# Performance work log

Measured on AMD Instinct MI355X. Metric: run time of the kernel, lower is better.

The kernel has to match this reference:

```python
import jax, jax.numpy as jnp
import numpy as np

Q, C, D = 4096, 4096, 1024
EPS = 1e-6  # torch.nn.PairwiseDistance default eps, added to (x1 - x2)


def _cdist_l2(a, b):
    # ||(a + EPS) - b||_2 for all pairs, via GEMM formulation.
    a = a + EPS
    sq = (jnp.sum(a * a, axis=1)[:, None]
          + jnp.sum(b * b, axis=1)[None, :]
          - 2.0 * a @ b.T)
    return jnp.sqrt(jnp.maximum(sq, 0.0))


def setup_inputs() -> dict:
    key = jax.random.key(0)
    k1, k2, k3, k4, k5, k6 = jax.random.split(key, 6)
    return {
        "context_rgb_features": jax.random.normal(k1, (C, D), dtype=jnp.float32),
        "context_flow_features": jax.random.normal(k2, (C, D), dtype=jnp.float32),
        "target_rgb_features": jax.random.normal(k3, (Q, D), dtype=jnp.float32),
        "target_flow_features": jax.random.normal(k4, (Q, D), dtype=jnp.float32),
        "c_r": jax.random.uniform(k5, (Q,), dtype=jnp.float32, minval=0.1, maxval=1.0),
        "c_f": jax.random.uniform(k6, (Q,), dtype=jnp.float32, minval=0.1, maxval=1.0),
    }


def reference(context_rgb_features, context_flow_features,
              target_rgb_features, target_flow_features, c_r, c_f):
    denom = c_r + c_f
    w_r = (c_r / denom)[:, None]   # [Q, 1]
    w_f = (c_f / denom)[:, None]
    d_rgb = _cdist_l2(target_rgb_features, context_rgb_features)    # [Q, C]
    d_flow = _cdist_l2(target_flow_features, context_flow_features)  # [Q, C]
    posterior = w_r * jnp.exp(-d_rgb) + w_f * jnp.exp(-d_flow)
    return posterior / jnp.sum(posterior, axis=1, keepdims=True)
```

## Files before the change

### kernel.cpp

```cpp
#include <hip/hip_runtime.h>
#include <hip/hip_bf16.h>

#define QN 4096
#define CN 4096
#define DN 1024
#define EPSV 1e-6f

#define BM 256
#define BN 256
#define TK 64
#define NT (DN / TK)
#define ATILE (BM * TK)
#define BUFE (2 * ATILE)

#define MATSZ ((size_t)QN * DN)

using bf16x8 = __attribute__((ext_vector_type(8))) __bf16;
using f32x4  = __attribute__((ext_vector_type(4))) float;

static __device__ __forceinline__ unsigned short f2bf_rne(float x) {
  unsigned int u = __float_as_uint(x);
  unsigned int r = (u + 0x7FFFu + ((u >> 16) & 1u)) >> 16;
  return (unsigned short)r;
}
static __device__ __forceinline__ float bf2f(unsigned short h) {
  return __uint_as_float(((unsigned int)h) << 16);
}

static __device__ __forceinline__ void gload_lds16(const unsigned short* g, unsigned short* l) {
  __builtin_amdgcn_global_load_lds(
      (const __attribute__((address_space(1))) unsigned int*)g,
      (__attribute__((address_space(3))) unsigned int*)l, 16, 0, 0);
}


__global__ void prep_kernel(const float* __restrict__ tgt_r, const float* __restrict__ tgt_f,
                            const float* __restrict__ ctx_r, const float* __restrict__ ctx_f,
                            unsigned short* __restrict__ ws16, float* __restrict__ norms) {
  const int row = blockIdx.x;
  const int mat = blockIdx.y;
  const int t = threadIdx.x;
  const float* src; float eps;
  switch (mat) {
    case 0:  src = tgt_r; eps = EPSV; break;
    case 1:  src = tgt_f; eps = EPSV; break;
    case 2:  src = ctx_r; eps = 0.f;  break;
    default: src = ctx_f; eps = 0.f;  break;
  }
  unsigned short* hi = ws16 + (size_t)mat * MATSZ;
  float* nrm = norms + (size_t)mat * QN;
  const size_t base = (size_t)row * DN;
  float4 v = ((const float4*)(src + base))[t];
  float a[4] = {v.x + eps, v.y + eps, v.z + eps, v.w + eps};
  float ss = 0.f;
  unsigned short hh[4];
#pragma unroll
  for (int k = 0; k < 4; ++k) {
    hh[k] = f2bf_rne(a[k]);
    float f = bf2f(hh[k]);
    ss += f * f;
  }
  ((ushort4*)(hi + base))[t] = make_ushort4(hh[0], hh[1], hh[2], hh[3]);
#pragma unroll
  for (int o = 32; o > 0; o >>= 1) ss += __shfl_down(ss, o);
  __shared__ float red[4];
  if ((t & 63) == 0) red[t >> 6] = ss;
  __syncthreads();
  if (t == 0) nrm[row] = red[0] + red[1] + red[2] + red[3];
}

template <bool ACCUM>
__global__ __launch_bounds__(512, 2)
void gemm_kernel(const unsigned short* __restrict__ A,
                 const unsigned short* __restrict__ B,
                 const float* __restrict__ tn,
                 const float* __restrict__ cn,
                 const float* __restrict__ cw_num,
                 const float* __restrict__ cw_oth,
                 float* __restrict__ out) {
  __shared__ unsigned short S[2 * BUFE];

  const int t = threadIdx.x;
  const int lane = t & 63;
  const int wid = t >> 6;
  const int wr = wid >> 2;
  const int wc = wid & 3;
  const int row0 = blockIdx.y * BM;
  const int col0 = blockIdx.x * BN;

  f32x4 acc[8][4];
#pragma unroll
  for (int m = 0; m < 8; ++m)
#pragma unroll
    for (int n = 0; n < 4; ++n)
      acc[m][n] = (f32x4){0.f, 0.f, 0.f, 0.f};

  const int srw = lane >> 3;
  const int sch = (lane & 7) ^ srw;
  const size_t src_off = (size_t)(wid * 8 + srw) * DN + sch * 8;
  const int ldsw = wid * 512;

  const unsigned short* pA = A + (size_t)row0 * DN + src_off;
  const unsigned short* pB = B + (size_t)col0 * DN + src_off;

  const int lr = lane & 15;
  const int lq = lane >> 4;
  const int sc0 = (lq ^ (lr & 7)) * 8;
  int ra[8], rb[4];
#pragma unroll
  for (int m = 0; m < 8; ++m) ra[m] = (wr * 128 + m * 16 + lr) * TK + sc0;
#pragma unroll
  for (int n = 0; n < 4; ++n) rb[n] = (wc * 64 + n * 16 + lr) * TK + sc0;
#define KS1(x) ((x) ^ 32)

#define STAGE(buf, kk)                                                        \
  do {                                                                        \
    unsigned short* Sb_ = S + (buf) * BUFE;                                   \
    _Pragma("unroll")                                                         \
    for (int i_ = 0; i_ < 4; ++i_) {                                          \
      const size_t g_ = (size_t)i_ * 64 * DN + (kk);                          \
      gload_lds16(pA + g_, Sb_ + i_ * 4096 + ldsw);                           \
      gload_lds16(pB + g_, Sb_ + ATILE + i_ * 4096 + ldsw);                   \
    }                                                                         \
  } while (0)

  STAGE(0, 0);
  __syncthreads();

  int cur = 0;
  for (int tt = 0; tt < NT; ++tt) {
    if (tt + 1 < NT) STAGE(cur ^ 1, (tt + 1) * TK);

    const unsigned short* Sb = S + cur * BUFE;
#pragma unroll
    for (int ksub = 0; ksub < 2; ++ksub) {
      bf16x8 a[8], b[4];
#pragma unroll
      for (int m = 0; m < 8; ++m)
        a[m] = *(const bf16x8*)(Sb + (ksub ? KS1(ra[m]) : ra[m]));
#pragma unroll
      for (int n = 0; n < 4; ++n)
        b[n] = *(const bf16x8*)(Sb + ATILE + (ksub ? KS1(rb[n]) : rb[n]));
#pragma unroll
      for (int m = 0; m < 8; ++m)
#pragma unroll
        for (int n = 0; n < 4; ++n)
          acc[m][n] = __builtin_amdgcn_mfma_f32_16x16x32_bf16(a[m], b[n], acc[m][n], 0, 0, 0);
    }

    __syncthreads();
    cur ^= 1;
  }

  float cnv[4];
  int ccv[4];
#pragma unroll
  for (int n = 0; n < 4; ++n) {
    ccv[n] = col0 + wc * 64 + n * 16 + lr;
    cnv[n] = cn[ccv[n]];
  }

#pragma unroll
  for (int m = 0; m < 8; ++m) {
#pragma unroll
    for (int r = 0; r < 4; ++r) {
      const int tq = row0 + wr * 128 + m * 16 + lq * 4 + r;
      const float tnq = tn[tq];
      const float num = cw_num[tq], oth = cw_oth[tq];
      const float wgt = num / (num + oth);
      float* orow = out + (size_t)tq * CN;
#pragma unroll
      for (int n = 0; n < 4; ++n) {
        const float sq = tnq + cnv[n] - 2.f * acc[m][n][r];
        const float d = sqrtf(fmaxf(sq, 0.f));
        const float e = wgt * __expf(-d);
        if (ACCUM) orow[ccv[n]] += e;
        else       orow[ccv[n]] = e;
      }
    }
  }
}

__global__ void norm_kernel(float* __restrict__ out) {
  const int row = blockIdx.x;
  const int t = threadIdx.x;
  float4* p = (float4*)(out + (size_t)row * CN);
  float4 v[4];
  float s = 0.f;
#pragma unroll
  for (int i = 0; i < 4; ++i) {
    v[i] = p[t + 256 * i];
    s += v[i].x + v[i].y + v[i].z + v[i].w;
  }
#pragma unroll
  for (int o = 32; o > 0; o >>= 1) s += __shfl_down(s, o);
  __shared__ float red[4];
  if ((t & 63) == 0) red[t >> 6] = s;
  __syncthreads();
  const float inv = 1.f / (red[0] + red[1] + red[2] + red[3]);
#pragma unroll
  for (int i = 0; i < 4; ++i) {
    v[i].x *= inv; v[i].y *= inv; v[i].z *= inv; v[i].w *= inv;
    p[t + 256 * i] = v[i];
  }
}

extern "C" void kernel_launch(void* const* d_in, const int* in_sizes, int n_in,
                              void* d_out, int out_size, void* d_ws, size_t ws_size,
                              hipStream_t stream) {
  const float* ctx_r = (const float*)d_in[0];
  const float* ctx_f = (const float*)d_in[1];
  const float* tgt_r = (const float*)d_in[2];
  const float* tgt_f = (const float*)d_in[3];
  const float* c_r   = (const float*)d_in[4];
  const float* c_f   = (const float*)d_in[5];
  float* out = (float*)d_out;
  unsigned short* ws16 = (unsigned short*)d_ws;
  float* norms = (float*)(ws16 + 4 * MATSZ);

  prep_kernel<<<dim3(QN, 4), 256, 0, stream>>>(tgt_r, tgt_f, ctx_r, ctx_f, ws16, norms);
  gemm_kernel<false><<<dim3(CN / BN, QN / BM), 512, 0, stream>>>(
      ws16 + 0 * MATSZ, ws16 + 2 * MATSZ, norms, norms + 2 * QN, c_r, c_f, out);
  gemm_kernel<true><<<dim3(CN / BN, QN / BM), 512, 0, stream>>>(
      ws16 + 1 * MATSZ, ws16 + 3 * MATSZ, norms + QN, norms + 3 * QN, c_f, c_r, out);
  norm_kernel<<<QN, 256, 0, stream>>>(out);
}
```

Baseline: 231.5 us.

## Split GEMM tile into quadrant sub-phases with interleaved half-tile prefetch

Restructures the bf16 MFMA main loop so each 256x256 block is computed as four 128x128 quadrants. Global-to-LDS loads of the next K-tile are issued as half-tiles between the quadrant phases, with explicit barriers, vmcnt/lgkmcnt waits, sched_barriers and setprio around the MFMA bursts. Each wave's 8x4 fragment layout becomes 2x2 quadrants of 4x2 fragments, which is meant to overlap LDS fills with compute and lower fragment register pressure. In exchange it adds many more barriers per K-tile and relies on hand-tuned wait counts for correctness.

```diff
diff --git a/kernel.cpp b/kernel.cpp
--- a/kernel.cpp
+++ b/kernel.cpp
@@ -8,10 +8,11 @@
 
 #define BM 256
 #define BN 256
-#define TK 64
-#define NT (DN / TK)
-#define ATILE (BM * TK)
-#define BUFE (2 * ATILE)
+#define BK 64
+#define NTILES (DN / BK)
+#define HALF 8192
+#define SLAB 16384
+#define BUF  32768
 
 #define MATSZ ((size_t)QN * DN)
 
@@ -78,107 +79,198 @@
                  const float* __restrict__ cw_num,
                  const float* __restrict__ cw_oth,
                  float* __restrict__ out) {
-  __shared__ unsigned short S[2 * BUFE];
+  __shared__ unsigned short S[2 * BUF];
 
   const int t = threadIdx.x;
   const int lane = t & 63;
   const int wid = t >> 6;
-  const int wr = wid >> 2;
-  const int wc = wid & 3;
+  const int wr2 = wid >> 2;
+  const int wc2 = wid & 3;
   const int row0 = blockIdx.y * BM;
   const int col0 = blockIdx.x * BN;
 
-  f32x4 acc[8][4];
-#pragma unroll
-  for (int m = 0; m < 8; ++m)
-#pragma unroll
-    for (int n = 0; n < 4; ++n)
-      acc[m][n] = (f32x4){0.f, 0.f, 0.f, 0.f};
+  f32x4 acc[2][2][4][2];
+#pragma unroll
+  for (int qa = 0; qa < 2; ++qa)
+#pragma unroll
+    for (int qb = 0; qb < 2; ++qb)
+#pragma unroll
+      for (int m = 0; m < 4; ++m)
+#pragma unroll
+        for (int n = 0; n < 2; ++n)
+          acc[qa][qb][m][n] = (f32x4){0.f, 0.f, 0.f, 0.f};
 
   const int srw = lane >> 3;
   const int sch = (lane & 7) ^ srw;
-  const size_t src_off = (size_t)(wid * 8 + srw) * DN + sch * 8;
-  const int ldsw = wid * 512;
-
-  const unsigned short* pA = A + (size_t)row0 * DN + src_off;
-  const unsigned short* pB = B + (size_t)col0 * DN + src_off;
+  const size_t so0 = (size_t)(wid * 8 + srw) * DN + sch * 8;
+  const size_t so1 = (size_t)(64 + wid * 8 + srw) * DN + sch * 8;
+  const int lo0 = (wid * 8) * 64;
+  const int lo1 = (64 + wid * 8) * 64;
+
+  const unsigned short* pA = A + (size_t)row0 * DN;
+  const unsigned short* pB = B + (size_t)col0 * DN;
 
   const int lr = lane & 15;
   const int lq = lane >> 4;
   const int sc0 = (lq ^ (lr & 7)) * 8;
-  int ra[8], rb[4];
-#pragma unroll
-  for (int m = 0; m < 8; ++m) ra[m] = (wr * 128 + m * 16 + lr) * TK + sc0;
-#pragma unroll
-  for (int n = 0; n < 4; ++n) rb[n] = (wc * 64 + n * 16 + lr) * TK + sc0;
-#define KS1(x) ((x) ^ 32)
-
-#define STAGE(buf, kk)                                                        \
+  int raoff[4][2], rboff[2][2];
+#pragma unroll
+  for (int m = 0; m < 4; ++m) {
+    const int base = (wr2 * 64 + m * 16 + lr) * BK + sc0;
+    raoff[m][0] = base; raoff[m][1] = base ^ 32;
+  }
+#pragma unroll
+  for (int n = 0; n < 2; ++n) {
+    const int base = (wc2 * 32 + n * 16 + lr) * BK + sc0;
+    rboff[n][0] = base; rboff[n][1] = base ^ 32;
+  }
+
+#define STAGEH(src, ldsbase, h, kk)                                           \
   do {                                                                        \
-    unsigned short* Sb_ = S + (buf) * BUFE;                                   \
-    _Pragma("unroll")                                                         \
-    for (int i_ = 0; i_ < 4; ++i_) {                                          \
-      const size_t g_ = (size_t)i_ * 64 * DN + (kk);                          \
-      gload_lds16(pA + g_, Sb_ + i_ * 4096 + ldsw);                           \
-      gload_lds16(pB + g_, Sb_ + ATILE + i_ * 4096 + ldsw);                   \
-    }                                                                         \
+    gload_lds16((src) + (size_t)((h) * 128) * DN + (kk) + so0,                \
+                (ldsbase) + (h) * HALF + lo0);                                \
+    gload_lds16((src) + (size_t)((h) * 128) * DN + (kk) + so1,                \
+                (ldsbase) + (h) * HALF + lo1);                                \
   } while (0)
 
-  STAGE(0, 0);
-  __syncthreads();
-
-  int cur = 0;
-  for (int tt = 0; tt < NT; ++tt) {
-    if (tt + 1 < NT) STAGE(cur ^ 1, (tt + 1) * TK);
-
-    const unsigned short* Sb = S + cur * BUFE;
-#pragma unroll
-    for (int ksub = 0; ksub < 2; ++ksub) {
-      bf16x8 a[8], b[4];
-#pragma unroll
-      for (int m = 0; m < 8; ++m)
-        a[m] = *(const bf16x8*)(Sb + (ksub ? KS1(ra[m]) : ra[m]));
-#pragma unroll
-      for (int n = 0; n < 4; ++n)
-        b[n] = *(const bf16x8*)(Sb + ATILE + (ksub ? KS1(rb[n]) : rb[n]));
-#pragma unroll
-      for (int m = 0; m < 8; ++m)
-#pragma unroll
-        for (int n = 0; n < 4; ++n)
-          acc[m][n] = __builtin_amdgcn_mfma_f32_16x16x32_bf16(a[m], b[n], acc[m][n], 0, 0, 0);
-    }
-
-    __syncthreads();
-    cur ^= 1;
-  }
-
-  float cnv[4];
-  int ccv[4];
-#pragma unroll
-  for (int n = 0; n < 4; ++n) {
-    ccv[n] = col0 + wc * 64 + n * 16 + lr;
-    cnv[n] = cn[ccv[n]];
-  }
-
-#pragma unroll
-  for (int m = 0; m < 8; ++m) {
-#pragma unroll
-    for (int r = 0; r < 4; ++r) {
-      const int tq = row0 + wr * 128 + m * 16 + lq * 4 + r;
-      const float tnq = tn[tq];
-      const float num = cw_num[tq], oth = cw_oth[tq];
-      const float wgt = num / (num + oth);
-      float* orow = out + (size_t)tq * CN;
-#pragma unroll
-      for (int n = 0; n < 4; ++n) {
-        const float sq = tnq + cnv[n] - 2.f * acc[m][n][r];
-        const float d = sqrtf(fmaxf(sq, 0.f));
-        const float e = wgt * __expf(-d);
-        if (ACCUM) orow[ccv[n]] += e;
-        else       orow[ccv[n]] = e;
-      }
-    }
-  }
+#define SBAR() __builtin_amdgcn_sched_barrier(0)
+#define BARRIER() do { SBAR(); __builtin_amdgcn_s_barrier(); SBAR(); } while (0)
+#define WAITLGKM0() do { asm volatile("s_waitcnt lgkmcnt(0)" ::: "memory"); SBAR(); } while (0)
+#define WAITVM4()   do { asm volatile("s_waitcnt vmcnt(4)" ::: "memory"); SBAR(); } while (0)
+
+  {
+    unsigned short* Na = S;
+    unsigned short* Nb = S + SLAB;
+    STAGEH(pA, Na, 0, 0);
+    STAGEH(pB, Nb, 0, 0);
+    STAGEH(pB, Nb, 1, 0);
+    STAGEH(pA, Na, 1, 0);
+    WAITVM4();
+    BARRIER();
+  }
+
+  bf16x8 Af[4][2], B0f[2][2], B1f[2][2];
+
+  for (int tt = 0; tt < NTILES; ++tt) {
+    const int b = tt & 1;
+    const unsigned short* Sa = S + b * BUF;
+    const unsigned short* Sb = S + b * BUF + SLAB;
+    unsigned short* Na = S + (b ^ 1) * BUF;
+    unsigned short* Nb = S + (b ^ 1) * BUF + SLAB;
+    const int kn = (tt + 1) * BK;
+    const bool notlast = (tt + 1 < NTILES);
+
+#pragma unroll
+    for (int m = 0; m < 4; ++m) {
+      Af[m][0] = *(const bf16x8*)(Sa + raoff[m][0]);
+      Af[m][1] = *(const bf16x8*)(Sa + raoff[m][1]);
+    }
+#pragma unroll
+    for (int n = 0; n < 2; ++n) {
+      B0f[n][0] = *(const bf16x8*)(Sb + rboff[n][0]);
+      B0f[n][1] = *(const bf16x8*)(Sb + rboff[n][1]);
+    }
+    if (notlast) STAGEH(pA, Na, 0, kn);
+    BARRIER();
+    WAITLGKM0();
+    __builtin_amdgcn_s_setprio(1);
+#pragma unroll
+    for (int m = 0; m < 4; ++m)
+#pragma unroll
+      for (int n = 0; n < 2; ++n) {
+        acc[0][0][m][n] = __builtin_amdgcn_mfma_f32_16x16x32_bf16(Af[m][0], B0f[n][0], acc[0][0][m][n], 0, 0, 0);
+        acc[0][0][m][n] = __builtin_amdgcn_mfma_f32_16x16x32_bf16(Af[m][1], B0f[n][1], acc[0][0][m][n], 0, 0, 0);
+      }
+    __builtin_amdgcn_s_setprio(0);
+    WAITVM4();
+    BARRIER();
+
+#pragma unroll
+    for (int n = 0; n < 2; ++n) {
+      B1f[n][0] = *(const bf16x8*)(Sb + HALF + rboff[n][0]);
+      B1f[n][1] = *(const bf16x8*)(Sb + HALF + rboff[n][1]);
+    }
+    if (notlast) STAGEH(pB, Nb, 0, kn);
+    BARRIER();
+    WAITLGKM0();
+    __builtin_amdgcn_s_setprio(1);
+#pragma unroll
+    for (int m = 0; m < 4; ++m)
+#pragma unroll
+      for (int n = 0; n < 2; ++n) {
+        acc[0][1][m][n] = __builtin_amdgcn_mfma_f32_16x16x32_bf16(Af[m][0], B1f[n][0], acc[0][1][m][n], 0, 0, 0);
+        acc[0][1][m][n] = __builtin_amdgcn_mfma_f32_16x16x32_bf16(Af[m][1], B1f[n][1], acc[0][1][m][n], 0, 0, 0);
+      }
+    __builtin_amdgcn_s_setprio(0);
+    WAITVM4();
+    BARRIER();
+
+#pragma unroll
+    for (int m = 0; m < 4; ++m) {
+      Af[m][0] = *(const bf16x8*)(Sa + HALF + raoff[m][0]);
+      Af[m][1] = *(const bf16x8*)(Sa + HALF + raoff[m][1]);
+    }
+    if (notlast) STAGEH(pB, Nb, 1, kn);
+    BARRIER();
+    WAITLGKM0();
+    __builtin_amdgcn_s_setprio(1);
+#pragma unroll
+    for (int m = 0; m < 4; ++m)
+#pragma unroll
+      for (int n = 0; n < 2; ++n) {
+        acc[1][1][m][n] = __builtin_amdgcn_mfma_f32_16x16x32_bf16(Af[m][0], B1f[n][0], acc[1][1][m][n], 0, 0, 0);
+        acc[1][1][m][n] = __builtin_amdgcn_mfma_f32_16x16x32_bf16(Af[m][1], B1f[n][1], acc[1][1][m][n], 0, 0, 0);
+      }
+    __builtin_amdgcn_s_setprio(0);
+    BARRIER();
+
+    if (notlast) STAGEH(pA, Na, 1, kn);
+    BARRIER();
+    __builtin_amdgcn_s_setprio(1);
+#pragma unroll
+    for (int m = 0; m < 4; ++m)
+#pragma unroll
+      for (int n = 0; n < 2; ++n) {
+        acc[1][0][m][n] = __builtin_amdgcn_mfma_f32_16x16x32_bf16(Af[m][0], B0f[n][0], acc[1][0][m][n], 0, 0, 0);
+        acc[1][0][m][n] = __builtin_amdgcn_mfma_f32_16x16x32_bf16(Af[m][1], B0f[n][1], acc[1][0][m][n], 0, 0, 0);
+      }
+    __builtin_amdgcn_s_setprio(0);
+    WAITVM4();
+    BARRIER();
+  }
+
+  float cnv[2][2];
+  int ccv[2][2];
+#pragma unroll
+  for (int qb = 0; qb < 2; ++qb)
+#pragma unroll
+    for (int n = 0; n < 2; ++n) {
+      ccv[qb][n] = col0 + qb * 128 + wc2 * 32 + n * 16 + lr;
+      cnv[qb][n] = cn[ccv[qb][n]];
+    }
+
+#pragma unroll
+  for (int qa = 0; qa < 2; ++qa)
+#pragma unroll
+    for (int m = 0; m < 4; ++m)
+#pragma unroll
+      for (int r = 0; r < 4; ++r) {
+        const int tq = row0 + qa * 128 + wr2 * 64 + m * 16 + lq * 4 + r;
+        const float tnq = tn[tq];
+        const float num = cw_num[tq], oth = cw_oth[tq];
+        const float wgt = num / (num + oth);
+        float* orow = out + (size_t)tq * CN;
+#pragma unroll
+        for (int qb = 0; qb < 2; ++qb)
+#pragma unroll
+          for (int n = 0; n < 2; ++n) {
+            const float sq = tnq + cnv[qb][n] - 2.f * acc[qa][qb][m][n][r];
+            const float d = sqrtf(fmaxf(sq, 0.f));
+            const float e = wgt * __expf(-d);
+            if (ACCUM) orow[ccv[qb][n]] += e;
+            else       orow[ccv[qb][n]] = e;
+          }
+      }
 }
 
 __global__ void norm_kernel(float* __restrict__ out) {
```

Measured after the change: 232.8 us. About the same (+0.6%).
